# Optimization experiments

Measured on AMD Instinct MI355X. Metric: run time of the kernel, lower is better.

## Reference

```python
import jax, jax.numpy as jnp
import numpy as np

HEADS = 16
HEAD_DIM = 1024 // HEADS  # 64
SCALE = float(np.sqrt(HEAD_DIM))  # math.sqrt(features // heads)


def setup_inputs() -> dict:
    key = jax.random.key(0)
    ks = jax.random.split(key, 6)
    n, m, d, c = 2048, 2048, 1024, 768
    return {
        "x": jax.random.normal(ks[0], (n, d), dtype=jnp.float32),
        "ctx": jax.random.normal(ks[1], (m, c), dtype=jnp.float32),
        "Wq": jax.random.normal(ks[2], (d, d), dtype=jnp.float32) * (1.0 / np.sqrt(d)),
        "Wk": jax.random.normal(ks[3], (c, d), dtype=jnp.float32) * (1.0 / np.sqrt(c)),
        "Wv": jax.random.normal(ks[4], (c, d), dtype=jnp.float32) * (1.0 / np.sqrt(c)),
        "Wo": jax.random.normal(ks[5], (d, d), dtype=jnp.float32) * (1.0 / np.sqrt(d)),
    }


def reference(x, ctx, Wq, Wk, Wv, Wo):
    n, d = x.shape
    q = (x @ Wq).reshape(n, HEADS, HEAD_DIM).transpose(1, 0, 2)      # h n d
    k = (ctx @ Wk).reshape(-1, HEADS, HEAD_DIM).transpose(1, 0, 2)   # h m d
    v = (ctx @ Wv).reshape(-1, HEADS, HEAD_DIM).transpose(1, 0, 2)   # h m d
    scores = jnp.einsum("hnd,hmd->hnm", q, k) / SCALE
    attn = jax.nn.softmax(scores, axis=-1)
    out = jnp.einsum("hnm,hmd->hnd", attn, v)                        # h n d
    out = out.transpose(1, 0, 2).reshape(n, d)                       # n (h d)
    return out @ Wo
```

## Files before the change

kernel.cpp:

```cpp
#include <hip/hip_runtime.h>
#include <hip/hip_bf16.h>
#include <stdint.h>

typedef unsigned short bfu;
typedef __attribute__((ext_vector_type(8))) short short8;
typedef __attribute__((ext_vector_type(4))) float f32x4;

__device__ __forceinline__ bfu f2bf(float f) {
  union { float f; uint32_t u; } v; v.f = f;
  uint32_t r = (v.u + 0x7fffu + ((v.u >> 16) & 1u)) >> 16;
  return (bfu)r;
}

__device__ __forceinline__ void gload16(const void* g, void* l) {
  __builtin_amdgcn_global_load_lds((const __attribute__((address_space(1))) void*)g,
                                   (__attribute__((address_space(3))) void*)l, 16, 0, 0);
}

__device__ __forceinline__ void conv_body(const float* __restrict__ in, bfu* __restrict__ out,
                                          int i) {
  const float4* p = (const float4*)in + (size_t)i * 2;
  float4 a = p[0], b = p[1];
  union { bfu h[8]; uint4 v; } o;
  o.h[0] = f2bf(a.x); o.h[1] = f2bf(a.y); o.h[2] = f2bf(a.z); o.h[3] = f2bf(a.w);
  o.h[4] = f2bf(b.x); o.h[5] = f2bf(b.y); o.h[6] = f2bf(b.z); o.h[7] = f2bf(b.w);
  ((uint4*)out)[i] = o.v;
}

__device__ __forceinline__ void trans_body(const float* __restrict__ W, bfu* __restrict__ WT,
                                           int Kd, int n0, int k0) {
  __shared__ float tile[32][33];
  const int tx = threadIdx.x & 31, ty = threadIdx.x >> 5;
#pragma unroll
  for (int i = 0; i < 32; i += 8)
    tile[ty + i][tx] = W[(size_t)(k0 + ty + i) * 1024 + n0 + tx];
  __syncthreads();
#pragma unroll
  for (int i = 0; i < 32; i += 8)
    WT[(size_t)(n0 + ty + i) * Kd + k0 + tx] = f2bf(tile[tx][ty + i]);
}

__global__ __launch_bounds__(256) void prep_kernel(
    const float* __restrict__ x, const float* __restrict__ ctx,
    const float* __restrict__ Wq, const float* __restrict__ Wk,
    const float* __restrict__ Wv, const float* __restrict__ Wo,
    bfu* xb, bfu* ctxb, bfu* WTq, bfu* WTk, bfu* WTv, bfu* WTo) {
  int b = blockIdx.x;
  if (b < 1024)       conv_body(x, xb, b * 256 + threadIdx.x);
  else if (b < 1792)  conv_body(ctx, ctxb, (b - 1024) * 256 + threadIdx.x);
  else if (b < 2816) { b -= 1792; trans_body(Wq, WTq, 1024, (b & 31) * 32, (b >> 5) * 32); }
  else if (b < 3584) { b -= 2816; trans_body(Wk, WTk, 768, (b & 31) * 32, (b >> 5) * 32); }
  else if (b < 4352) { b -= 3584; trans_body(Wv, WTv, 768, (b & 31) * 32, (b >> 5) * 32); }
  else               { b -= 4352; trans_body(Wo, WTo, 1024, (b & 31) * 32, (b >> 5) * 32); }
}

typedef bfu AsArr[2][4][128][8];
typedef bfu BsArr[2][4][64][8];

__device__ __forceinline__ void gemm_body(AsArr& As2, BsArr& Bs2,
    const bfu* __restrict__ A, const bfu* __restrict__ BT,
    bfu* __restrict__ Cb, float* __restrict__ Cf,
    int N, int K, float scale, int m0, int n0) {
  const int tid = threadIdx.x, lane = tid & 63, wave = tid >> 6;
  const int g = lane >> 4, c = lane & 15;
  const int wm = wave * 32;
  const int nt = K / 32;

  auto stage = [&](int buf, int kt) {
#pragma unroll
    for (int u = 0; u < 3; ++u) {
      int idx = wave * 3 + u;
      if (idx < 8) {
        int g2 = idx & 3, rb = idx >> 2;
        gload16(&A[(size_t)(m0 + rb * 64 + lane) * K + kt + g2 * 8], &As2[buf][g2][rb * 64][0]);
      } else {
        int g2 = idx - 8;
        gload16(&BT[(size_t)(n0 + lane) * K + kt + g2 * 8], &Bs2[buf][g2][0][0]);
      }
    }
  };

  f32x4 acc[2][4] = {};
  stage(0, 0);
  for (int t = 0; t < nt; ++t) {
    __syncthreads();
    if (t + 1 < nt) stage((t + 1) & 1, (t + 1) * 32);
    const int b = t & 1;
    short8 af[2], bfr[4];
#pragma unroll
    for (int i = 0; i < 2; ++i) af[i] = *(const short8*)&As2[b][g][wm + i * 16 + c][0];
#pragma unroll
    for (int j = 0; j < 4; ++j) bfr[j] = *(const short8*)&Bs2[b][g][j * 16 + c][0];
#pragma unroll
    for (int i = 0; i < 2; ++i)
#pragma unroll
      for (int j = 0; j < 4; ++j)
        acc[i][j] = __builtin_amdgcn_mfma_f32_16x16x32_bf16(af[i], bfr[j], acc[i][j], 0, 0, 0);
  }
#pragma unroll
  for (int i = 0; i < 2; ++i)
#pragma unroll
    for (int j = 0; j < 4; ++j) {
      int row = m0 + wm + i * 16 + g * 4;
      int col = n0 + j * 16 + c;
#pragma unroll
      for (int r = 0; r < 4; ++r) {
        float v = acc[i][j][r] * scale;
        if (Cb) Cb[(size_t)(row + r) * N + col] = f2bf(v);
        else    Cf[(size_t)(row + r) * N + col] = v;
      }
    }
}

__global__ __launch_bounds__(256) void gemm3_kernel(
    const bfu* __restrict__ xb, const bfu* __restrict__ WTq, bfu* __restrict__ Qb,
    const bfu* __restrict__ ctxb, const bfu* __restrict__ WTk, bfu* __restrict__ Kb,
    const bfu* __restrict__ WTv, bfu* __restrict__ Vtb) {
  __shared__ alignas(16) bfu As2[2][4][128][8];
  __shared__ alignas(16) bfu Bs2[2][4][64][8];
  int bid = blockIdx.x, p = bid >> 8, r = bid & 255;
  if (p == 0)
    gemm_body(As2, Bs2, xb, WTq, Qb, nullptr, 1024, 1024, 0.125f, (r >> 4) * 128, (r & 15) * 64);
  else if (p == 1)
    gemm_body(As2, Bs2, ctxb, WTk, Kb, nullptr, 1024, 768, 1.0f, (r >> 4) * 128, (r & 15) * 64);
  else
    gemm_body(As2, Bs2, WTv, ctxb, Vtb, nullptr, 2048, 768, 1.0f, (r >> 5) * 128, (r & 31) * 64);
}

__global__ __launch_bounds__(256) void gemmo_kernel(const bfu* __restrict__ AO,
                                                    const bfu* __restrict__ WTo,
                                                    float* __restrict__ out) {
  __shared__ alignas(16) bfu As2[2][4][128][8];
  __shared__ alignas(16) bfu Bs2[2][4][64][8];
  int bid = blockIdx.x;
  gemm_body(As2, Bs2, AO, WTo, nullptr, out, 1024, 1024, 1.0f, (bid >> 4) * 128, (bid & 15) * 64);
}

__global__ __launch_bounds__(256) void attn_kernel(
    const bfu* __restrict__ Q, const bfu* __restrict__ Kmat,
    const bfu* __restrict__ Vt, bfu* __restrict__ O) {
  __shared__ alignas(16) bfu Ks[3][8][64][8];
  __shared__ alignas(16) bfu Vs[3][8][64][8];
  __shared__ alignas(16) bfu Ps[4][16][72];
  const int tid = threadIdx.x, wave = tid >> 6, lane = tid & 63;
  const int g = lane >> 4, c = lane & 15;
  const int h = blockIdx.y;
  const int q0 = blockIdx.x * 64 + wave * 16;
  const int col0 = h * 64;

  short8 qf0 = *(const short8*)&Q[(size_t)(q0 + c) * 1024 + col0 + g * 8];
  short8 qf1 = *(const short8*)&Q[(size_t)(q0 + c) * 1024 + col0 + 32 + g * 8];

  short8 ones;
#pragma unroll
  for (int e = 0; e < 8; ++e) ones[e] = (short)0x3F80;

  f32x4 o_acc[4] = {};
  f32x4 lacc = {};

  auto stage = [&](int buf, int kv0) {
#pragma unroll
    for (int u = 0; u < 4; ++u) {
      int idx = wave * 4 + u;
      if (idx < 8)
        gload16(&Kmat[(size_t)(kv0 + lane) * 1024 + col0 + idx * 8], &Ks[buf][idx][0][0]);
      else
        gload16(&Vt[(size_t)(col0 + lane) * 2048 + kv0 + (idx - 8) * 8], &Vs[buf][idx - 8][0][0]);
    }
  };

  stage(0, 0);
  stage(1, 64);
  for (int t = 0; t < 32; ++t) {
    const int b = t % 3;
    asm volatile("s_waitcnt vmcnt(4) lgkmcnt(0)\n\ts_barrier" ::: "memory");
    __builtin_amdgcn_sched_barrier(0);
    f32x4 s[4] = {};
    __builtin_amdgcn_s_setprio(1);
#pragma unroll
    for (int f = 0; f < 4; ++f) {
      short8 kf0 = *(const short8*)&Ks[b][g][f * 16 + c][0];
      short8 kf1 = *(const short8*)&Ks[b][4 + g][f * 16 + c][0];
      s[f] = __builtin_amdgcn_mfma_f32_16x16x32_bf16(qf0, kf0, s[f], 0, 0, 0);
      s[f] = __builtin_amdgcn_mfma_f32_16x16x32_bf16(qf1, kf1, s[f], 0, 0, 0);
    }
    __builtin_amdgcn_s_setprio(0);
#pragma unroll
    for (int f = 0; f < 4; ++f)
#pragma unroll
      for (int j = 0; j < 4; ++j)
        Ps[wave][g * 4 + j][f * 16 + c] = f2bf(__expf(s[f][j]));
    asm volatile("s_waitcnt lgkmcnt(0)\n\ts_barrier" ::: "memory");
    __builtin_amdgcn_sched_barrier(0);
    { int tn = t + 2; stage(tn % 3, (tn & 31) * 64); }
    __builtin_amdgcn_s_setprio(1);
#pragma unroll
    for (int kc = 0; kc < 2; ++kc) {
      short8 pf = *(const short8*)&Ps[wave][c][kc * 32 + g * 8];
      lacc = __builtin_amdgcn_mfma_f32_16x16x32_bf16(pf, ones, lacc, 0, 0, 0);
#pragma unroll
      for (int fd = 0; fd < 4; ++fd) {
        short8 vf = *(const short8*)&Vs[b][kc * 4 + g][fd * 16 + c][0];
        o_acc[fd] = __builtin_amdgcn_mfma_f32_16x16x32_bf16(pf, vf, o_acc[fd], 0, 0, 0);
      }
    }
    __builtin_amdgcn_s_setprio(0);
  }
#pragma unroll
  for (int fd = 0; fd < 4; ++fd)
#pragma unroll
    for (int j = 0; j < 4; ++j) {
      float v = o_acc[fd][j] / lacc[j];
      O[(size_t)(q0 + g * 4 + j) * 1024 + col0 + fd * 16 + c] = f2bf(v);
    }
}

extern "C" void kernel_launch(void* const* d_in, const int* in_sizes, int n_in,
                              void* d_out, int out_size, void* d_ws, size_t ws_size,
                              hipStream_t stream) {
  const float* x   = (const float*)d_in[0];
  const float* ctx = (const float*)d_in[1];
  const float* Wq  = (const float*)d_in[2];
  const float* Wk  = (const float*)d_in[3];
  const float* Wv  = (const float*)d_in[4];
  const float* Wo  = (const float*)d_in[5];
  float* out = (float*)d_out;

  bfu* ws   = (bfu*)d_ws;
  bfu* xb   = ws;
  bfu* WTk  = xb + 2048 * 1024;
  bfu* WTv  = WTk + 1024 * 768;
  bfu* WTo  = WTv + 1024 * 768;
  bfu* Qb   = WTo + 1024 * 1024;
  bfu* Kb   = Qb + 2048 * 1024;
  bfu* Vtb  = Kb + 2048 * 1024;
  bfu* WTq  = (bfu*)d_out;
  bfu* ctxb = WTq + 1024 * 1024;

  dim3 blk(256);
  prep_kernel<<<5376, blk, 0, stream>>>(x, ctx, Wq, Wk, Wv, Wo, xb, ctxb, WTq, WTk, WTv, WTo);
  gemm3_kernel<<<768, blk, 0, stream>>>(xb, WTq, Qb, ctxb, WTk, Kb, WTv, Vtb);
  attn_kernel<<<dim3(32, 16), blk, 0, stream>>>(Qb, Kb, Vtb, xb);
  gemmo_kernel<<<256, blk, 0, stream>>>(xb, WTo, out);
}
```

Measured before the change: 117.4 us.

## Process two query tiles per wave in attention to reuse K/V fragments

Each wave now handles 32 query rows instead of 16, so every K and V fragment loaded from shared memory feeds two sets of MFMAs, and the grid is halved to 256 blocks. The pipeline also drops from triple buffering with hand-placed waitcnt/barrier sequences to double buffering with plain __syncthreads. This cuts LDS reads and global K/V traffic per query, but leaves fewer blocks (256, roughly one per CU) and loses the deeper prefetch, so load latency may be exposed.

Result: no change. 117.1 us (-0.3%).

```diff
diff --git a/kernel.cpp b/kernel.cpp
--- a/kernel.cpp
+++ b/kernel.cpp
@@ -139,24 +139,28 @@
 __global__ __launch_bounds__(256) void attn_kernel(
     const bfu* __restrict__ Q, const bfu* __restrict__ Kmat,
     const bfu* __restrict__ Vt, bfu* __restrict__ O) {
-  __shared__ alignas(16) bfu Ks[3][8][64][8];
-  __shared__ alignas(16) bfu Vs[3][8][64][8];
-  __shared__ alignas(16) bfu Ps[4][16][72];
+  __shared__ alignas(16) bfu Ks[2][8][64][8];
+  __shared__ alignas(16) bfu Vs[2][8][64][8];
+  __shared__ alignas(16) bfu Ps[4][32][72];
   const int tid = threadIdx.x, wave = tid >> 6, lane = tid & 63;
   const int g = lane >> 4, c = lane & 15;
   const int h = blockIdx.y;
-  const int q0 = blockIdx.x * 64 + wave * 16;
+  const int qbase = blockIdx.x * 128 + wave * 32;
   const int col0 = h * 64;
 
-  short8 qf0 = *(const short8*)&Q[(size_t)(q0 + c) * 1024 + col0 + g * 8];
-  short8 qf1 = *(const short8*)&Q[(size_t)(q0 + c) * 1024 + col0 + 32 + g * 8];
+  short8 qf[2][2];
+#pragma unroll
+  for (int qi = 0; qi < 2; ++qi) {
+    qf[qi][0] = *(const short8*)&Q[(size_t)(qbase + qi * 16 + c) * 1024 + col0 + g * 8];
+    qf[qi][1] = *(const short8*)&Q[(size_t)(qbase + qi * 16 + c) * 1024 + col0 + 32 + g * 8];
+  }
 
   short8 ones;
 #pragma unroll
   for (int e = 0; e < 8; ++e) ones[e] = (short)0x3F80;
 
-  f32x4 o_acc[4] = {};
-  f32x4 lacc = {};
+  f32x4 o_acc[2][4] = {};
+  f32x4 lacc[2] = {};
 
   auto stage = [&](int buf, int kv0) {
 #pragma unroll
@@ -170,49 +174,62 @@
   };
 
   stage(0, 0);
-  stage(1, 64);
   for (int t = 0; t < 32; ++t) {
-    const int b = t % 3;
-    asm volatile("s_waitcnt vmcnt(4) lgkmcnt(0)\n\ts_barrier" ::: "memory");
-    __builtin_amdgcn_sched_barrier(0);
-    f32x4 s[4] = {};
+    __syncthreads();
+    if (t < 31) stage((t + 1) & 1, (t + 1) * 64);
+    const int b = t & 1;
+    short8 kf[4][2];
+#pragma unroll
+    for (int f = 0; f < 4; ++f) {
+      kf[f][0] = *(const short8*)&Ks[b][g][f * 16 + c][0];
+      kf[f][1] = *(const short8*)&Ks[b][4 + g][f * 16 + c][0];
+    }
+#pragma unroll
+    for (int qi = 0; qi < 2; ++qi) {
+      f32x4 s[4] = {};
+      __builtin_amdgcn_s_setprio(1);
+#pragma unroll
+      for (int f = 0; f < 4; ++f) {
+        s[f] = __builtin_amdgcn_mfma_f32_16x16x32_bf16(qf[qi][0], kf[f][0], s[f], 0, 0, 0);
+        s[f] = __builtin_amdgcn_mfma_f32_16x16x32_bf16(qf[qi][1], kf[f][1], s[f], 0, 0, 0);
+      }
+      __builtin_amdgcn_s_setprio(0);
+#pragma unroll
+      for (int f = 0; f < 4; ++f)
+#pragma unroll
+        for (int j = 0; j < 4; ++j)
+          Ps[wave][qi * 16 + g * 4 + j][f * 16 + c] = f2bf(__expf(s[f][j]));
+    }
+    __syncthreads();
+    short8 vf[2][4];
+#pragma unroll
+    for (int kc = 0; kc < 2; ++kc)
+#pragma unroll
+      for (int fd = 0; fd < 4; ++fd)
+        vf[kc][fd] = *(const short8*)&Vs[b][kc * 4 + g][fd * 16 + c][0];
     __builtin_amdgcn_s_setprio(1);
 #pragma unroll
-    for (int f = 0; f < 4; ++f) {
-      short8 kf0 = *(const short8*)&Ks[b][g][f * 16 + c][0];
-      short8 kf1 = *(const short8*)&Ks[b][4 + g][f * 16 + c][0];
-      s[f] = __builtin_amdgcn_mfma_f32_16x16x32_bf16(qf0, kf0, s[f], 0, 0, 0);
-      s[f] = __builtin_amdgcn_mfma_f32_16x16x32_bf16(qf1, kf1, s[f], 0, 0, 0);
-    }
-    __builtin_amdgcn_s_setprio(0);
-#pragma unroll
-    for (int f = 0; f < 4; ++f)
-#pragma unroll
-      for (int j = 0; j < 4; ++j)
-        Ps[wave][g * 4 + j][f * 16 + c] = f2bf(__expf(s[f][j]));
-    asm volatile("s_waitcnt lgkmcnt(0)\n\ts_barrier" ::: "memory");
-    __builtin_amdgcn_sched_barrier(0);
-    { int tn = t + 2; stage(tn % 3, (tn & 31) * 64); }
-    __builtin_amdgcn_s_setprio(1);
-#pragma unroll
-    for (int kc = 0; kc < 2; ++kc) {
-      short8 pf = *(const short8*)&Ps[wave][c][kc * 32 + g * 8];
-      lacc = __builtin_amdgcn_mfma_f32_16x16x32_bf16(pf, ones, lacc, 0, 0, 0);
-#pragma unroll
-      for (int fd = 0; fd < 4; ++fd) {
-        short8 vf = *(const short8*)&Vs[b][kc * 4 + g][fd * 16 + c][0];
-        o_acc[fd] = __builtin_amdgcn_mfma_f32_16x16x32_bf16(pf, vf, o_acc[fd], 0, 0, 0);
+    for (int qi = 0; qi < 2; ++qi) {
+#pragma unroll
+      for (int kc = 0; kc < 2; ++kc) {
+        short8 pf = *(const short8*)&Ps[wave][qi * 16 + c][kc * 32 + g * 8];
+        lacc[qi] = __builtin_amdgcn_mfma_f32_16x16x32_bf16(pf, ones, lacc[qi], 0, 0, 0);
+#pragma unroll
+        for (int fd = 0; fd < 4; ++fd)
+          o_acc[qi][fd] = __builtin_amdgcn_mfma_f32_16x16x32_bf16(pf, vf[kc][fd], o_acc[qi][fd], 0, 0, 0);
       }
     }
     __builtin_amdgcn_s_setprio(0);
   }
 #pragma unroll
-  for (int fd = 0; fd < 4; ++fd)
-#pragma unroll
-    for (int j = 0; j < 4; ++j) {
-      float v = o_acc[fd][j] / lacc[j];
-      O[(size_t)(q0 + g * 4 + j) * 1024 + col0 + fd * 16 + c] = f2bf(v);
-    }
+  for (int qi = 0; qi < 2; ++qi)
+#pragma unroll
+    for (int fd = 0; fd < 4; ++fd)
+#pragma unroll
+      for (int j = 0; j < 4; ++j) {
+        float v = o_acc[qi][fd][j] / lacc[qi][j];
+        O[(size_t)(qbase + qi * 16 + g * 4 + j) * 1024 + col0 + fd * 16 + c] = f2bf(v);
+      }
 }
 
 extern "C" void kernel_launch(void* const* d_in, const int* in_sizes, int n_in,
@@ -240,6 +257,6 @@
   dim3 blk(256);
   prep_kernel<<<5376, blk, 0, stream>>>(x, ctx, Wq, Wk, Wv, Wo, xb, ctxb, WTq, WTk, WTv, WTo);
   gemm3_kernel<<<768, blk, 0, stream>>>(xb, WTq, Qb, ctxb, WTk, Kb, WTv, Vtb);
-  attn_kernel<<<dim3(32, 16), blk, 0, stream>>>(Qb, Kb, Vtb, xb);
+  attn_kernel<<<dim3(16, 16), blk, 0, stream>>>(Qb, Kb, Vtb, xb);
   gemmo_kernel<<<256, blk, 0, stream>>>(xb, WTo, out);
 }
```

## Split attention QK^T across waves by key tile and share P through LDS

Applied to the files above, without the earlier changes.

Each wave now keeps Q fragments for all 64 query rows in registers and computes scores for its own 16-key slice, so K fragments are read from LDS once per wave instead of four times. The per-wave P buffers become one shared 64x64 tile that every wave reads back for its own query rows in the PV step. The triple-buffered K/V pipeline with explicit vmcnt waits is replaced by a double buffer with plain __syncthreads. This trades fewer LDS reads of K for more Q registers, extra block-wide barriers, and a shallower prefetch pipeline.

Measured after the change: 114.6 us. 1.02x faster.

```diff
diff --git a/kernel.cpp b/kernel.cpp
--- a/kernel.cpp
+++ b/kernel.cpp
@@ -139,17 +139,21 @@
 __global__ __launch_bounds__(256) void attn_kernel(
     const bfu* __restrict__ Q, const bfu* __restrict__ Kmat,
     const bfu* __restrict__ Vt, bfu* __restrict__ O) {
-  __shared__ alignas(16) bfu Ks[3][8][64][8];
-  __shared__ alignas(16) bfu Vs[3][8][64][8];
-  __shared__ alignas(16) bfu Ps[4][16][72];
+  __shared__ alignas(16) bfu Ks[2][8][64][8];
+  __shared__ alignas(16) bfu Vs[2][8][64][8];
+  __shared__ alignas(16) bfu Ps[64][72];
   const int tid = threadIdx.x, wave = tid >> 6, lane = tid & 63;
   const int g = lane >> 4, c = lane & 15;
   const int h = blockIdx.y;
-  const int q0 = blockIdx.x * 64 + wave * 16;
+  const int qblk = blockIdx.x * 64;
   const int col0 = h * 64;
 
-  short8 qf0 = *(const short8*)&Q[(size_t)(q0 + c) * 1024 + col0 + g * 8];
-  short8 qf1 = *(const short8*)&Q[(size_t)(q0 + c) * 1024 + col0 + 32 + g * 8];
+  short8 qf[4][2];
+#pragma unroll
+  for (int qt = 0; qt < 4; ++qt) {
+    qf[qt][0] = *(const short8*)&Q[(size_t)(qblk + qt * 16 + c) * 1024 + col0 + g * 8];
+    qf[qt][1] = *(const short8*)&Q[(size_t)(qblk + qt * 16 + c) * 1024 + col0 + 32 + g * 8];
+  }
 
   short8 ones;
 #pragma unroll
@@ -170,33 +174,30 @@
   };
 
   stage(0, 0);
-  stage(1, 64);
   for (int t = 0; t < 32; ++t) {
-    const int b = t % 3;
-    asm volatile("s_waitcnt vmcnt(4) lgkmcnt(0)\n\ts_barrier" ::: "memory");
-    __builtin_amdgcn_sched_barrier(0);
+    __syncthreads();
+    if (t < 31) stage((t + 1) & 1, (t + 1) * 64);
+    const int b = t & 1;
+    short8 kf0 = *(const short8*)&Ks[b][g][wave * 16 + c][0];
+    short8 kf1 = *(const short8*)&Ks[b][4 + g][wave * 16 + c][0];
     f32x4 s[4] = {};
     __builtin_amdgcn_s_setprio(1);
 #pragma unroll
-    for (int f = 0; f < 4; ++f) {
-      short8 kf0 = *(const short8*)&Ks[b][g][f * 16 + c][0];
-      short8 kf1 = *(const short8*)&Ks[b][4 + g][f * 16 + c][0];
-      s[f] = __builtin_amdgcn_mfma_f32_16x16x32_bf16(qf0, kf0, s[f], 0, 0, 0);
-      s[f] = __builtin_amdgcn_mfma_f32_16x16x32_bf16(qf1, kf1, s[f], 0, 0, 0);
+    for (int qt = 0; qt < 4; ++qt) {
+      s[qt] = __builtin_amdgcn_mfma_f32_16x16x32_bf16(qf[qt][0], kf0, s[qt], 0, 0, 0);
+      s[qt] = __builtin_amdgcn_mfma_f32_16x16x32_bf16(qf[qt][1], kf1, s[qt], 0, 0, 0);
     }
     __builtin_amdgcn_s_setprio(0);
 #pragma unroll
-    for (int f = 0; f < 4; ++f)
+    for (int qt = 0; qt < 4; ++qt)
 #pragma unroll
       for (int j = 0; j < 4; ++j)
-        Ps[wave][g * 4 + j][f * 16 + c] = f2bf(__expf(s[f][j]));
-    asm volatile("s_waitcnt lgkmcnt(0)\n\ts_barrier" ::: "memory");
-    __builtin_amdgcn_sched_barrier(0);
-    { int tn = t + 2; stage(tn % 3, (tn & 31) * 64); }
+        Ps[qt * 16 + g * 4 + j][wave * 16 + c] = f2bf(__expf(s[qt][j]));
+    __syncthreads();
     __builtin_amdgcn_s_setprio(1);
 #pragma unroll
     for (int kc = 0; kc < 2; ++kc) {
-      short8 pf = *(const short8*)&Ps[wave][c][kc * 32 + g * 8];
+      short8 pf = *(const short8*)&Ps[wave * 16 + c][kc * 32 + g * 8];
       lacc = __builtin_amdgcn_mfma_f32_16x16x32_bf16(pf, ones, lacc, 0, 0, 0);
 #pragma unroll
       for (int fd = 0; fd < 4; ++fd) {
@@ -206,6 +207,7 @@
     }
     __builtin_amdgcn_s_setprio(0);
   }
+  const int q0 = qblk + wave * 16;
 #pragma unroll
   for (int fd = 0; fd < 4; ++fd)
 #pragma unroll
```
